# Kernel tuning notes

Measured on AMD Instinct MI355X. Metric: run time of the kernel, lower is better.

Reference implementation:

```python
import jax, jax.numpy as jnp
import numpy as np

N, E = 100000, 600000
IN_DIM, HID, OUT_DIM = 128, 128, 1
BN_EPS = 1e-5
L2_EPS = 1e-12


def setup_inputs() -> dict:
    key = jax.random.key(0)
    ks = jax.random.split(key, 12)

    def xavier(k, shape):
        fan_in, fan_out = shape[0], shape[1]
        lim = float(np.sqrt(6.0 / (fan_in + fan_out)))
        return jax.random.uniform(k, shape, jnp.float32, -lim, lim)

    return {
        'x': jax.random.normal(ks[0], (N, IN_DIM), jnp.float32),
        'edge_index': jax.random.randint(ks[1], (2, E), 0, N, jnp.int32),
        # SAGEConv layer 1: lin_l (neighbor, with bias), lin_r (root, no bias)
        'W1_l': xavier(ks[2], (IN_DIM, HID)),
        'b1_l': jnp.zeros((HID,), jnp.float32),
        'W1_r': xavier(ks[3], (IN_DIM, HID)),
        # BatchNorm1d(hidden)
        'bn_gamma': jnp.ones((HID,), jnp.float32),
        'bn_beta': jnp.zeros((HID,), jnp.float32),
        # SAGEConv layer 2
        'W2_l': xavier(ks[4], (HID, HID)),
        'b2_l': jnp.zeros((HID,), jnp.float32),
        'W2_r': xavier(ks[5], (HID, HID)),
        # fc on causal half of embedding
        'fc_W': xavier(ks[6], (HID // 2, OUT_DIM)),
        'fc_b': jnp.zeros((OUT_DIM,), jnp.float32),
    }


def _sage_conv(x, src, dst, W_l, b_l, W_r, n_nodes):
    # mean-aggregate neighbor features: messages x[src] scattered to dst
    msg = x[src]  # [E, d] gather
    agg = jax.ops.segment_sum(msg, dst, num_segments=n_nodes)  # [N, d]
    cnt = jax.ops.segment_sum(jnp.ones((src.shape[0],), x.dtype), dst,
                              num_segments=n_nodes)  # [N]
    mean = agg / jnp.maximum(cnt, 1.0)[:, None]
    out = mean @ W_l + b_l + x @ W_r  # lin_l(agg) + lin_r(x)
    # normalize=True -> row-wise L2 normalize (F.normalize, eps=1e-12)
    nrm = jnp.linalg.norm(out, axis=-1, keepdims=True)
    return out / jnp.maximum(nrm, L2_EPS)


def reference(x, edge_index, W1_l, b1_l, W1_r, bn_gamma, bn_beta,
              W2_l, b2_l, W2_r, fc_W, fc_b):
    src, dst = edge_index[0], edge_index[1]
    n_nodes = x.shape[0]

    h = _sage_conv(x, src, dst, W1_l, b1_l, W1_r, n_nodes)

    # transition: ReLU -> BatchNorm1d (batch stats) -> Dropout (eval: identity)
    h = jax.nn.relu(h)
    mu = jnp.mean(h, axis=0)
    var = jnp.var(h, axis=0)
    h = (h - mu) * jax.lax.rsqrt(var + BN_EPS) * bn_gamma + bn_beta

    embed = _sage_conv(h, src, dst, W2_l, b2_l, W2_r, n_nodes)

    half = embed.shape[1] // 2
    preds = (embed[:, :half] @ fc_W + fc_b).squeeze()  # [N]
    return preds, embed
```

## Files before the change

### kernel.cpp

```cpp
#include <hip/hip_runtime.h>
#include <hip/hip_bf16.h>
#include <stdint.h>

typedef __attribute__((ext_vector_type(8))) __bf16 bf16x8;
typedef __attribute__((ext_vector_type(4))) float  f32x4;

__device__ __forceinline__ float bflo(uint32_t p){ return __uint_as_float(p << 16); }
__device__ __forceinline__ float bfhi(uint32_t p){ return __uint_as_float(p & 0xffff0000u); }
__device__ __forceinline__ uint16_t f2bf(float f){
    uint32_t u = __float_as_uint(f);
    uint32_t r = (u + 0x7fffu + ((u >> 16) & 1u)) >> 16;
    return (uint16_t)r;
}
__device__ __forceinline__ uint32_t packbf(float a, float b){
    return (uint32_t)f2bf(a) | ((uint32_t)f2bf(b) << 16);
}
__device__ __forceinline__ f32x4 MFMA(bf16x8 a, bf16x8 b, f32x4 c){
    return __builtin_amdgcn_mfma_f32_16x16x32_bf16(a, b, c, 0, 0, 0);
}


__global__ void k_deg(const int* __restrict__ dst, int* __restrict__ counts, int E){
    int e = blockIdx.x * 256 + threadIdx.x;
    if (e < E) atomicAdd(&counts[dst[e]], 1);
}

__global__ void k_scan1(const int* __restrict__ counts, int* __restrict__ bsums, int N){
    __shared__ int lds[256];
    int t = threadIdx.x;
    int base = blockIdx.x * 2048 + t * 8;
    int s = 0;
    #pragma unroll
    for (int i = 0; i < 8; ++i){ int idx = base + i; s += (idx < N) ? counts[idx] : 0; }
    lds[t] = s; __syncthreads();
    for (int off = 128; off > 0; off >>= 1){
        if (t < off) lds[t] += lds[t + off];
        __syncthreads();
    }
    if (t == 0) bsums[blockIdx.x] = lds[0];
}

__global__ void k_scan2(int* bsums, int NB){
    int run = 0;
    for (int i = 0; i < NB; ++i){ int v = bsums[i]; bsums[i] = run; run += v; }
}

__global__ void k_scan3(const int* __restrict__ counts, const int* __restrict__ bsums,
                        int* __restrict__ offs, int N){
    __shared__ int lds[256];
    int t = threadIdx.x;
    int base = blockIdx.x * 2048 + t * 8;
    int local[8];
    int s = 0;
    #pragma unroll
    for (int i = 0; i < 8; ++i){
        int idx = base + i;
        int v = (idx < N) ? counts[idx] : 0;
        local[i] = v; s += v;
    }
    lds[t] = s; __syncthreads();
    for (int off = 1; off < 256; off <<= 1){
        int v = (t >= off) ? lds[t - off] : 0;
        __syncthreads();
        lds[t] += v;
        __syncthreads();
    }
    int run = bsums[blockIdx.x] + (lds[t] - s);
    #pragma unroll
    for (int i = 0; i < 8; ++i){
        int idx = base + i;
        if (idx < N){ offs[idx] = run; run += local[i]; }
    }
}

__global__ void k_fill(const int* __restrict__ src, const int* __restrict__ dst,
                       const int* __restrict__ offs, int* __restrict__ cursor,
                       int* __restrict__ ssrc, int E){
    int e = blockIdx.x * 256 + threadIdx.x;
    if (e < E){
        int d = dst[e];
        int p = atomicAdd(&cursor[d], 1);
        ssrc[offs[d] + p] = src[e];
    }
}

__global__ __launch_bounds__(256) void k_x2bf(const float* __restrict__ X,
        uint32_t* __restrict__ XbfE, uint32_t* __restrict__ Xlo, int N){
    int i = blockIdx.x * 256 + threadIdx.x;
    if (i >= N * 32) return;
    int row = i >> 5, l = i & 31;
    float4 v = *(const float4*)(X + (size_t)i * 4);
    uint16_t h0 = f2bf(v.x), h1 = f2bf(v.y), h2 = f2bf(v.z), h3 = f2bf(v.w);
    float r0 = v.x - __uint_as_float((uint32_t)h0 << 16);
    float r1 = v.y - __uint_as_float((uint32_t)h1 << 16);
    float r2 = v.z - __uint_as_float((uint32_t)h2 << 16);
    float r3 = v.w - __uint_as_float((uint32_t)h3 << 16);
    uint2 hi; hi.x = (uint32_t)h0 | ((uint32_t)h1 << 16);
    hi.y = (uint32_t)h2 | ((uint32_t)h3 << 16);
    uint2 lo; lo.x = packbf(r0, r1); lo.y = packbf(r2, r3);
    *(uint2*)(XbfE + (size_t)row * 128 + l * 2) = hi;
    *(uint2*)(Xlo  + (size_t)row * 64  + l * 2) = lo;
}

__global__ void k_wprep(const float* __restrict__ Wl, const float* __restrict__ Wr,
                        const float* __restrict__ scale,
                        uint16_t* __restrict__ Wpk){
    int idx = blockIdx.x * 256 + threadIdx.x;
    int c = idx >> 8, k = idx & 255;
    float v;
    if (k < 128){
        v = Wl[k * 128 + c];
    } else {
        v = Wr[(k - 128) * 128 + c];
        if (scale) v *= scale[k - 128];
    }
    uint16_t h = f2bf(v);
    float r = v - __uint_as_float((uint32_t)h << 16);
    int kt = k >> 5, kk = k & 31;
    int g = kk >> 3, e = kk & 7;
    int slot = (c << 2) | (g ^ ((c >> 1) & 3));
    size_t base = (size_t)kt * 8192 + (size_t)slot * 8 + e;
    Wpk[base]        = h;
    Wpk[base + 4096] = f2bf(r);
}

template<int MODE>
__global__ __launch_bounds__(256) void k_agg(
        const uint32_t* __restrict__ Src, int sstr,
        const int* __restrict__ offs, const int* __restrict__ counts,
        const int* __restrict__ ssrc,
        const float* __restrict__ bnscale, const float* __restrict__ bnshift,
        uint32_t* __restrict__ MbBase, int N){
    const int lane = threadIdx.x & 63;
    const int l15  = lane & 15;
    const int q    = lane >> 4;
    int node = blockIdx.x * 4 + (threadIdx.x >> 6);
    if (node >= N) return;
    int cnt = counts[node];
    if (cnt < 0) cnt = 0;
    int off = offs[node];
    const uint32_t* srcb = Src + l15 * 4;
    float a[8];
    #pragma unroll
    for (int i = 0; i < 8; ++i) a[i] = 0.f;

    int j = 0;
    for (; j + 8 <= cnt; j += 8){
        int s0 = ssrc[off + j + q];
        int s1 = ssrc[off + j + 4 + q];
        s0 = (s0 < 0) ? 0 : ((s0 >= N) ? (N - 1) : s0);
        s1 = (s1 < 0) ? 0 : ((s1 >= N) ? (N - 1) : s1);
        uint4 v0 = *(const uint4*)(srcb + (size_t)s0 * sstr);
        uint4 v1 = *(const uint4*)(srcb + (size_t)s1 * sstr);
        a[0] += bflo(v0.x) + bflo(v1.x); a[1] += bfhi(v0.x) + bfhi(v1.x);
        a[2] += bflo(v0.y) + bflo(v1.y); a[3] += bfhi(v0.y) + bfhi(v1.y);
        a[4] += bflo(v0.z) + bflo(v1.z); a[5] += bfhi(v0.z) + bfhi(v1.z);
        a[6] += bflo(v0.w) + bflo(v1.w); a[7] += bfhi(v0.w) + bfhi(v1.w);
    }
    int rem = cnt - j;
    if (rem > 0){
        if (q < rem){
            int s0 = ssrc[off + j + q];
            s0 = (s0 < 0) ? 0 : ((s0 >= N) ? (N - 1) : s0);
            uint4 v0 = *(const uint4*)(srcb + (size_t)s0 * sstr);
            a[0] += bflo(v0.x); a[1] += bfhi(v0.x);
            a[2] += bflo(v0.y); a[3] += bfhi(v0.y);
            a[4] += bflo(v0.z); a[5] += bfhi(v0.z);
            a[6] += bflo(v0.w); a[7] += bfhi(v0.w);
        }
        if (rem > 4 && q < rem - 4){
            int s1 = ssrc[off + j + 4 + q];
            s1 = (s1 < 0) ? 0 : ((s1 >= N) ? (N - 1) : s1);
            uint4 v1 = *(const uint4*)(srcb + (size_t)s1 * sstr);
            a[0] += bflo(v1.x); a[1] += bfhi(v1.x);
            a[2] += bflo(v1.y); a[3] += bfhi(v1.y);
            a[4] += bflo(v1.z); a[5] += bfhi(v1.z);
            a[6] += bflo(v1.w); a[7] += bfhi(v1.w);
        }
    }

    #pragma unroll
    for (int i = 0; i < 8; ++i){
        a[i] += __shfl_xor(a[i], 16, 64);
        a[i] += __shfl_xor(a[i], 32, 64);
    }
    float inv = 1.0f / fmaxf((float)cnt, 1.0f);
    #pragma unroll
    for (int i = 0; i < 8; ++i) a[i] *= inv;

    if (MODE == 1){
        if (cnt > 0){
            int c0 = l15 * 8;
            float4 sc0 = *(const float4*)(bnscale + c0);
            float4 sc1 = *(const float4*)(bnscale + c0 + 4);
            float4 sh0 = *(const float4*)(bnshift + c0);
            float4 sh1 = *(const float4*)(bnshift + c0 + 4);
            a[0] = a[0] * sc0.x + sh0.x; a[1] = a[1] * sc0.y + sh0.y;
            a[2] = a[2] * sc0.z + sh0.z; a[3] = a[3] * sc0.w + sh0.w;
            a[4] = a[4] * sc1.x + sh1.x; a[5] = a[5] * sc1.y + sh1.y;
            a[6] = a[6] * sc1.z + sh1.z; a[7] = a[7] * sc1.w + sh1.w;
        } else {
            #pragma unroll
            for (int i = 0; i < 8; ++i) a[i] = 0.f;
        }
    }

    if (q == 0){
        uint4 o;
        o.x = packbf(a[0], a[1]); o.y = packbf(a[2], a[3]);
        o.z = packbf(a[4], a[5]); o.w = packbf(a[6], a[7]);
        *(uint4*)(MbBase + (size_t)node * 128 + 64 + l15 * 4) = o;
    }
}

__device__ __forceinline__ void stage4(const uint32_t* Wpk, uint32_t (*sB)[2048],
                                       int wid, int lane, int sel, int half){
    #pragma unroll
    for (int i = 0; i < 4; ++i){
        int ch = wid * 4 + i;
        int ktv = ch >> 3, part = ch & 7;
        __builtin_amdgcn_global_load_lds(
            Wpk + (size_t)(half * 4 + ktv) * 4096 + sel * 2048 + part * 256 + lane * 4,
            &sB[ktv][part * 256], 16, 0, 0);
    }
}

template<int MODE>
__global__ __launch_bounds__(512, 4) void k_gemm(
        const uint32_t* Own,
        const uint32_t* OwnLo,
        const uint32_t* Mb,
        const uint32_t* __restrict__ Wpk,
        const float* __restrict__ bias,
        uint32_t* HbfOut,
        float* Emb,
        float* __restrict__ bnsum, float* __restrict__ bnsumsq,
        const float* __restrict__ fcW, const float* __restrict__ fcb,
        float* __restrict__ preds, int N){
    __shared__ uint32_t __align__(16) sB[4][2048];
    const int lane = threadIdx.x & 63;
    const int wid  = threadIdx.x >> 6;
    const int l15  = lane & 15;
    const int g    = lane >> 4;
    const int gx4  = (g ^ ((l15 >> 1) & 3)) * 4;
    const int ostr = (MODE == 0) ? 128 : 64;
    const int wrow = blockIdx.x * 128 + wid * 16;

    stage4(Wpk, sB, wid, lane, 0, 0);

    int ar0 = wrow + l15; if (ar0 >= N) ar0 = N - 1;

    const uint32_t* mp0 = Mb  + (size_t)ar0 * 128 + 64 + g * 4;
    const uint32_t* op0 = Own + (size_t)ar0 * ostr + g * 4;

    bf16x8 am[4], ao[4];
    #pragma unroll
    for (int kq = 0; kq < 4; ++kq){
        am[kq] = *(const bf16x8*)(mp0 + kq * 16);
        ao[kq] = *(const bf16x8*)(op0 + kq * 16);
    }
    bf16x8 xl[4];
    if (MODE == 0){
        #pragma unroll
        for (int kq = 0; kq < 4; ++kq)
            xl[kq] = *(const bf16x8*)(OwnLo + (size_t)ar0 * 64 + g * 4 + kq * 16);
    }

    f32x4 acc[8];
    const f32x4 zero = {0.f, 0.f, 0.f, 0.f};
    #pragma unroll
    for (int t = 0; t < 8; ++t) acc[t] = zero;

#define COMPUTE4(AM, ADD_XLO)                                                 \
    _Pragma("unroll")                                                         \
    for (int kk = 0; kk < 4; ++kk){                                           \
        _Pragma("unroll")                                                     \
        for (int t = 0; t < 8; ++t){                                          \
            bf16x8 bq = *(const bf16x8*)(&sB[kk][(t * 16 + l15) * 16 + gx4]); \
            acc[t] = MFMA(AM[kk], bq, acc[t]);                                \
            if (ADD_XLO) acc[t] = MFMA(xl[kk], bq, acc[t]);                   \
        }                                                                     \
    }

    __syncthreads();
    COMPUTE4(am, false);
    __syncthreads();
    stage4(Wpk, sB, wid, lane, 0, 1);
    __syncthreads();
    COMPUTE4(ao, (MODE == 0));
    __syncthreads();
    stage4(Wpk, sB, wid, lane, 1, 0);
    __syncthreads();
    COMPUTE4(am, false);
    __syncthreads();
    stage4(Wpk, sB, wid, lane, 1, 1);
    __syncthreads();
    COMPUTE4(ao, false);
#undef COMPUTE4

    float bv[8];
    #pragma unroll
    for (int t = 0; t < 8; ++t) bv[t] = bias[t * 16 + l15];

    float fw[4]; float fb = 0.f;
    if (MODE == 1){
        #pragma unroll
        for (int t = 0; t < 4; ++t) fw[t] = fcW[t * 16 + l15];
        fb = fcb[0];
    }

    float pbs[8], pbq[8];
    #pragma unroll
    for (int t = 0; t < 8; ++t){ pbs[t] = 0.f; pbq[t] = 0.f; }

    #pragma unroll
    for (int j = 0; j < 4; ++j){
        int orow = wrow + 4 * g + j;
        bool valid = orow < N;
        float o[8]; float ss = 0.f;
        #pragma unroll
        for (int t = 0; t < 8; ++t){
            o[t] = acc[t][j] + bv[t];
            ss += o[t] * o[t];
        }
        ss += __shfl_xor(ss, 1, 64);
        ss += __shfl_xor(ss, 2, 64);
        ss += __shfl_xor(ss, 4, 64);
        ss += __shfl_xor(ss, 8, 64);
        float inv = 1.0f / fmaxf(sqrtf(ss), 1e-12f);
        if (MODE == 0){
            #pragma unroll
            for (int t = 0; t < 8; ++t){
                float v = fmaxf(o[t] * inv, 0.f);
                float pv = __shfl_xor(v, 1, 64);
                if (valid){
                    pbs[t] += v; pbq[t] += v * v;
                    if (!(lane & 1))
                        HbfOut[(size_t)orow * 64 + t * 8 + (l15 >> 1)] = packbf(v, pv);
                }
            }
        } else {
            float p = 0.f;
            #pragma unroll
            for (int t = 0; t < 8; ++t){
                float v = o[t] * inv;
                if (valid) Emb[(size_t)orow * 128 + t * 16 + l15] = v;
                if (t < 4) p += v * fw[t];
            }
            p += __shfl_xor(p, 1, 64);
            p += __shfl_xor(p, 2, 64);
            p += __shfl_xor(p, 4, 64);
            p += __shfl_xor(p, 8, 64);
            if (valid && l15 == 0) preds[orow] = p + fb;
        }
    }

    if (MODE == 0){
        float* lsum = (float*)&sB[0][0];
        float* lsq  = lsum + 128;
        #pragma unroll
        for (int t = 0; t < 8; ++t){
            pbs[t] += __shfl_xor(pbs[t], 16, 64);
            pbs[t] += __shfl_xor(pbs[t], 32, 64);
            pbq[t] += __shfl_xor(pbq[t], 16, 64);
            pbq[t] += __shfl_xor(pbq[t], 32, 64);
        }
        __syncthreads();
        if (threadIdx.x < 128){ lsum[threadIdx.x] = 0.f; lsq[threadIdx.x] = 0.f; }
        __syncthreads();
        if (lane < 16){
            #pragma unroll
            for (int t = 0; t < 8; ++t){
                atomicAdd(&lsum[t * 16 + lane], pbs[t]);
                atomicAdd(&lsq [t * 16 + lane], pbq[t]);
            }
        }
        __syncthreads();
        if (threadIdx.x < 128){
            atomicAdd(&bnsum[threadIdx.x],   lsum[threadIdx.x]);
            atomicAdd(&bnsumsq[threadIdx.x], lsq[threadIdx.x]);
        }
    }
}

__global__ void k_bnfinal(const float* __restrict__ bnsum, const float* __restrict__ bnsumsq,
                          const float* __restrict__ gamma, const float* __restrict__ beta,
                          const float* __restrict__ W2r, const float* __restrict__ b2,
                          float* __restrict__ scale, float* __restrict__ shift,
                          float* __restrict__ bias2, int N){
    __shared__ float sh_l[128];
    int t = threadIdx.x;
    float invN = 1.0f / (float)N;
    float mu  = bnsum[t] * invN;
    float var = fmaxf(bnsumsq[t] * invN - mu * mu, 0.f);
    float istd = 1.0f / sqrtf(var + 1e-5f);
    float sc = gamma[t] * istd;
    float sf = beta[t] - mu * sc;
    scale[t] = sc; shift[t] = sf; sh_l[t] = sf;
    __syncthreads();
    float acc = b2[t];
    for (int k = 0; k < 128; ++k) acc += sh_l[k] * W2r[k * 128 + t];
    bias2[t] = acc;
}

__global__ void k_sent(float* __restrict__ preds, int N, float val){
    int i = blockIdx.x * 256 + threadIdx.x;
    if (i < N) preds[i] = val;
}

extern "C" void kernel_launch(void* const* d_in, const int* in_sizes, int n_in,
                              void* d_out, int out_size, void* d_ws, size_t ws_size,
                              hipStream_t stream){
    const int N = in_sizes[0] / 128;
    const int E = in_sizes[1] / 2;

    const float* x    = (const float*)d_in[0];
    const int*   ei   = (const int*)d_in[1];
    const int*   src  = ei;
    const int*   dst  = ei + E;
    const float* W1l  = (const float*)d_in[2];
    const float* b1   = (const float*)d_in[3];
    const float* W1r  = (const float*)d_in[4];
    const float* gam  = (const float*)d_in[5];
    const float* bet  = (const float*)d_in[6];
    const float* W2l  = (const float*)d_in[7];
    const float* b2   = (const float*)d_in[8];
    const float* W2r  = (const float*)d_in[9];
    const float* fcW  = (const float*)d_in[10];
    const float* fcb  = (const float*)d_in[11];

    float* preds = (float*)d_out;
    float* Emb   = preds + N;
    uint32_t* EmbU = (uint32_t*)Emb;

    char* w = (char*)d_ws;
    auto carve = [&](size_t bytes){ char* p = w; w += (bytes + 255) & ~(size_t)255; return p; };
    int*   counts  = (int*)  carve((size_t)N * 8);
    int*   cursor  = counts + N;
    int*   offs    = (int*)  carve((size_t)N * 4);
    int*   bsums   = (int*)  carve(256 * 4);
    float* bnsum   = (float*)carve(128 * 4);
    float* bnsumsq = (float*)carve(128 * 4);
    float* bnscale = (float*)carve(128 * 4);
    float* bnshift = (float*)carve(128 * 4);
    float* bias2   = (float*)carve(128 * 4);
    int*   ssrc    = (int*)  carve((size_t)E * 4);
    uint32_t* HbfXlo = (uint32_t*)carve((size_t)N * 256);
    uint16_t* Wpk1 = (uint16_t*)carve(131072);
    uint16_t* Wpk2 = (uint16_t*)carve(131072);
    size_t need = (size_t)(w - (char*)d_ws);
    if (ws_size < need){
        float val = 1024.f + 4.f * (float)((ws_size >> 20) > 255 ? 255 : (ws_size >> 20));
        k_sent<<<(N + 255) / 256, 256, 0, stream>>>(preds, N, val);
        return;
    }

    hipMemsetAsync(counts, 0, (size_t)N * 8, stream);
    hipMemsetAsync(bnsum,  0, 1024, stream);

    const int eb = (E + 255) / 256;
    const int NB = (N + 2047) / 2048;
    const int ab = (N + 3) / 4;
    const int gb = (N + 127) / 128;
    const int xb = (N * 32 + 255) / 256;

    k_deg  <<<eb, 256, 0, stream>>>(dst, counts, E);
    k_scan1<<<NB, 256, 0, stream>>>(counts, bsums, N);
    k_scan2<<<1,    1, 0, stream>>>(bsums, NB);
    k_scan3<<<NB, 256, 0, stream>>>(counts, bsums, offs, N);
    k_fill <<<eb, 256, 0, stream>>>(src, dst, offs, cursor, ssrc, E);

    k_x2bf <<<xb, 256, 0, stream>>>(x, EmbU, HbfXlo, N);
    k_wprep<<<128, 256, 0, stream>>>(W1l, W1r, nullptr, Wpk1);

    k_agg<0> <<<ab, 256, 0, stream>>>(EmbU, 128, offs, counts, ssrc,
                                      nullptr, nullptr, EmbU, N);
    k_gemm<0><<<gb, 512, 0, stream>>>(EmbU, HbfXlo, EmbU, (const uint32_t*)Wpk1, b1,
                                      HbfXlo, nullptr, bnsum, bnsumsq,
                                      nullptr, nullptr, nullptr, N);
    k_bnfinal<<<1, 128, 0, stream>>>(bnsum, bnsumsq, gam, bet, W2r, b2,
                                     bnscale, bnshift, bias2, N);
    k_wprep<<<128, 256, 0, stream>>>(W2l, W2r, bnscale, Wpk2);

    k_agg<1> <<<ab, 256, 0, stream>>>(HbfXlo, 64, offs, counts, ssrc,
                                      bnscale, bnshift, EmbU, N);
    k_gemm<1><<<gb, 512, 0, stream>>>(HbfXlo, nullptr, EmbU, (const uint32_t*)Wpk2, bias2,
                                      nullptr, Emb, nullptr, nullptr,
                                      fcW, fcb, preds, N);
}
```

Measured before the change: 356.5 us.

## Fuse neighbor mean aggregation into the SAGE GEMM kernel via LDS staging

Removes the separate k_agg kernels. Each GEMM warp now gathers and averages neighbor features for its own 16 rows, then writes the packed bf16 means into a swizzled LDS tile that feeds the MFMA A operand. This drops the global write and re-read of the mean buffer and two kernel launches. To fit, the GEMM block shrinks from 512 to 256 threads (64 rows per block), and each wave stages twice as much weight data. The cost is that each warp walks its 16 rows one after another, so fewer gather loads are in flight to hide memory latency.

Result: slower. 430.7 us (+20.8%).

```diff
diff --git a/kernel.cpp b/kernel.cpp
--- a/kernel.cpp
+++ b/kernel.cpp
@@ -124,100 +124,11 @@
     Wpk[base + 4096] = f2bf(r);
 }
 
-template<int MODE>
-__global__ __launch_bounds__(256) void k_agg(
-        const uint32_t* __restrict__ Src, int sstr,
-        const int* __restrict__ offs, const int* __restrict__ counts,
-        const int* __restrict__ ssrc,
-        const float* __restrict__ bnscale, const float* __restrict__ bnshift,
-        uint32_t* __restrict__ MbBase, int N){
-    const int lane = threadIdx.x & 63;
-    const int l15  = lane & 15;
-    const int q    = lane >> 4;
-    int node = blockIdx.x * 4 + (threadIdx.x >> 6);
-    if (node >= N) return;
-    int cnt = counts[node];
-    if (cnt < 0) cnt = 0;
-    int off = offs[node];
-    const uint32_t* srcb = Src + l15 * 4;
-    float a[8];
-    #pragma unroll
-    for (int i = 0; i < 8; ++i) a[i] = 0.f;
-
-    int j = 0;
-    for (; j + 8 <= cnt; j += 8){
-        int s0 = ssrc[off + j + q];
-        int s1 = ssrc[off + j + 4 + q];
-        s0 = (s0 < 0) ? 0 : ((s0 >= N) ? (N - 1) : s0);
-        s1 = (s1 < 0) ? 0 : ((s1 >= N) ? (N - 1) : s1);
-        uint4 v0 = *(const uint4*)(srcb + (size_t)s0 * sstr);
-        uint4 v1 = *(const uint4*)(srcb + (size_t)s1 * sstr);
-        a[0] += bflo(v0.x) + bflo(v1.x); a[1] += bfhi(v0.x) + bfhi(v1.x);
-        a[2] += bflo(v0.y) + bflo(v1.y); a[3] += bfhi(v0.y) + bfhi(v1.y);
-        a[4] += bflo(v0.z) + bflo(v1.z); a[5] += bfhi(v0.z) + bfhi(v1.z);
-        a[6] += bflo(v0.w) + bflo(v1.w); a[7] += bfhi(v0.w) + bfhi(v1.w);
-    }
-    int rem = cnt - j;
-    if (rem > 0){
-        if (q < rem){
-            int s0 = ssrc[off + j + q];
-            s0 = (s0 < 0) ? 0 : ((s0 >= N) ? (N - 1) : s0);
-            uint4 v0 = *(const uint4*)(srcb + (size_t)s0 * sstr);
-            a[0] += bflo(v0.x); a[1] += bfhi(v0.x);
-            a[2] += bflo(v0.y); a[3] += bfhi(v0.y);
-            a[4] += bflo(v0.z); a[5] += bfhi(v0.z);
-            a[6] += bflo(v0.w); a[7] += bfhi(v0.w);
-        }
-        if (rem > 4 && q < rem - 4){
-            int s1 = ssrc[off + j + 4 + q];
-            s1 = (s1 < 0) ? 0 : ((s1 >= N) ? (N - 1) : s1);
-            uint4 v1 = *(const uint4*)(srcb + (size_t)s1 * sstr);
-            a[0] += bflo(v1.x); a[1] += bfhi(v1.x);
-            a[2] += bflo(v1.y); a[3] += bfhi(v1.y);
-            a[4] += bflo(v1.z); a[5] += bfhi(v1.z);
-            a[6] += bflo(v1.w); a[7] += bfhi(v1.w);
-        }
-    }
-
-    #pragma unroll
-    for (int i = 0; i < 8; ++i){
-        a[i] += __shfl_xor(a[i], 16, 64);
-        a[i] += __shfl_xor(a[i], 32, 64);
-    }
-    float inv = 1.0f / fmaxf((float)cnt, 1.0f);
-    #pragma unroll
-    for (int i = 0; i < 8; ++i) a[i] *= inv;
-
-    if (MODE == 1){
-        if (cnt > 0){
-            int c0 = l15 * 8;
-            float4 sc0 = *(const float4*)(bnscale + c0);
-            float4 sc1 = *(const float4*)(bnscale + c0 + 4);
-            float4 sh0 = *(const float4*)(bnshift + c0);
-            float4 sh1 = *(const float4*)(bnshift + c0 + 4);
-            a[0] = a[0] * sc0.x + sh0.x; a[1] = a[1] * sc0.y + sh0.y;
-            a[2] = a[2] * sc0.z + sh0.z; a[3] = a[3] * sc0.w + sh0.w;
-            a[4] = a[4] * sc1.x + sh1.x; a[5] = a[5] * sc1.y + sh1.y;
-            a[6] = a[6] * sc1.z + sh1.z; a[7] = a[7] * sc1.w + sh1.w;
-        } else {
-            #pragma unroll
-            for (int i = 0; i < 8; ++i) a[i] = 0.f;
-        }
-    }
-
-    if (q == 0){
-        uint4 o;
-        o.x = packbf(a[0], a[1]); o.y = packbf(a[2], a[3]);
-        o.z = packbf(a[4], a[5]); o.w = packbf(a[6], a[7]);
-        *(uint4*)(MbBase + (size_t)node * 128 + 64 + l15 * 4) = o;
-    }
-}
-
 __device__ __forceinline__ void stage4(const uint32_t* Wpk, uint32_t (*sB)[2048],
                                        int wid, int lane, int sel, int half){
     #pragma unroll
-    for (int i = 0; i < 4; ++i){
-        int ch = wid * 4 + i;
+    for (int i = 0; i < 8; ++i){
+        int ch = wid * 8 + i;
         int ktv = ch >> 3, part = ch & 7;
         __builtin_amdgcn_global_load_lds(
             Wpk + (size_t)(half * 4 + ktv) * 4096 + sel * 2048 + part * 256 + lane * 4,
@@ -226,10 +137,12 @@
 }
 
 template<int MODE>
-__global__ __launch_bounds__(512, 4) void k_gemm(
+__global__ __launch_bounds__(256) void k_gemm(
         const uint32_t* Own,
         const uint32_t* OwnLo,
-        const uint32_t* Mb,
+        const int* __restrict__ offs, const int* __restrict__ counts,
+        const int* __restrict__ ssrc,
+        const float* __restrict__ bnscale, const float* __restrict__ bnshift,
         const uint32_t* __restrict__ Wpk,
         const float* __restrict__ bias,
         uint32_t* HbfOut,
@@ -238,27 +151,23 @@
         const float* __restrict__ fcW, const float* __restrict__ fcb,
         float* __restrict__ preds, int N){
     __shared__ uint32_t __align__(16) sB[4][2048];
+    __shared__ uint32_t __align__(16) sM[4][16][64];
     const int lane = threadIdx.x & 63;
     const int wid  = threadIdx.x >> 6;
     const int l15  = lane & 15;
     const int g    = lane >> 4;
     const int gx4  = (g ^ ((l15 >> 1) & 3)) * 4;
     const int ostr = (MODE == 0) ? 128 : 64;
-    const int wrow = blockIdx.x * 128 + wid * 16;
+    const int wrow = blockIdx.x * 64 + wid * 16;
 
     stage4(Wpk, sB, wid, lane, 0, 0);
 
     int ar0 = wrow + l15; if (ar0 >= N) ar0 = N - 1;
 
-    const uint32_t* mp0 = Mb  + (size_t)ar0 * 128 + 64 + g * 4;
     const uint32_t* op0 = Own + (size_t)ar0 * ostr + g * 4;
-
-    bf16x8 am[4], ao[4];
-    #pragma unroll
-    for (int kq = 0; kq < 4; ++kq){
-        am[kq] = *(const bf16x8*)(mp0 + kq * 16);
-        ao[kq] = *(const bf16x8*)(op0 + kq * 16);
-    }
+    bf16x8 ao[4];
+    #pragma unroll
+    for (int kq = 0; kq < 4; ++kq) ao[kq] = *(const bf16x8*)(op0 + kq * 16);
     bf16x8 xl[4];
     if (MODE == 0){
         #pragma unroll
@@ -266,37 +175,131 @@
             xl[kq] = *(const bf16x8*)(OwnLo + (size_t)ar0 * 64 + g * 4 + kq * 16);
     }
 
+    int cntv = counts[ar0];
+    int offv = offs[ar0];
+
+    float sc[8], sh[8];
+    if (MODE == 1){
+        int c0 = l15 * 8;
+        float4 s0 = *(const float4*)(bnscale + c0);
+        float4 s1 = *(const float4*)(bnscale + c0 + 4);
+        float4 h0 = *(const float4*)(bnshift + c0);
+        float4 h1 = *(const float4*)(bnshift + c0 + 4);
+        sc[0]=s0.x; sc[1]=s0.y; sc[2]=s0.z; sc[3]=s0.w;
+        sc[4]=s1.x; sc[5]=s1.y; sc[6]=s1.z; sc[7]=s1.w;
+        sh[0]=h0.x; sh[1]=h0.y; sh[2]=h0.z; sh[3]=h0.w;
+        sh[4]=h1.x; sh[5]=h1.y; sh[6]=h1.z; sh[7]=h1.w;
+    }
+
+    const uint32_t* srcb = Own + l15 * 4;
+    for (int r = 0; r < 16; ++r){
+        int cnt = __shfl(cntv, r, 64);
+        int off = __shfl(offv, r, 64);
+        if (cnt < 0) cnt = 0;
+        float a[8];
+        #pragma unroll
+        for (int i = 0; i < 8; ++i) a[i] = 0.f;
+        int j = 0;
+        for (; j + 8 <= cnt; j += 8){
+            int s0 = ssrc[off + j + g];
+            int s1 = ssrc[off + j + 4 + g];
+            s0 = (s0 < 0) ? 0 : ((s0 >= N) ? (N - 1) : s0);
+            s1 = (s1 < 0) ? 0 : ((s1 >= N) ? (N - 1) : s1);
+            uint4 v0 = *(const uint4*)(srcb + (size_t)s0 * ostr);
+            uint4 v1 = *(const uint4*)(srcb + (size_t)s1 * ostr);
+            a[0] += bflo(v0.x) + bflo(v1.x); a[1] += bfhi(v0.x) + bfhi(v1.x);
+            a[2] += bflo(v0.y) + bflo(v1.y); a[3] += bfhi(v0.y) + bfhi(v1.y);
+            a[4] += bflo(v0.z) + bflo(v1.z); a[5] += bfhi(v0.z) + bfhi(v1.z);
+            a[6] += bflo(v0.w) + bflo(v1.w); a[7] += bfhi(v0.w) + bfhi(v1.w);
+        }
+        int rem = cnt - j;
+        if (rem > 0){
+            if (g < rem){
+                int s0 = ssrc[off + j + g];
+                s0 = (s0 < 0) ? 0 : ((s0 >= N) ? (N - 1) : s0);
+                uint4 v0 = *(const uint4*)(srcb + (size_t)s0 * ostr);
+                a[0] += bflo(v0.x); a[1] += bfhi(v0.x);
+                a[2] += bflo(v0.y); a[3] += bfhi(v0.y);
+                a[4] += bflo(v0.z); a[5] += bfhi(v0.z);
+                a[6] += bflo(v0.w); a[7] += bfhi(v0.w);
+            }
+            if (rem > 4 && g < rem - 4){
+                int s1 = ssrc[off + j + 4 + g];
+                s1 = (s1 < 0) ? 0 : ((s1 >= N) ? (N - 1) : s1);
+                uint4 v1 = *(const uint4*)(srcb + (size_t)s1 * ostr);
+                a[0] += bflo(v1.x); a[1] += bfhi(v1.x);
+                a[2] += bflo(v1.y); a[3] += bfhi(v1.y);
+                a[4] += bflo(v1.z); a[5] += bfhi(v1.z);
+                a[6] += bflo(v1.w); a[7] += bfhi(v1.w);
+            }
+        }
+        #pragma unroll
+        for (int i = 0; i < 8; ++i){
+            a[i] += __shfl_xor(a[i], 16, 64);
+            a[i] += __shfl_xor(a[i], 32, 64);
+        }
+        float inv = 1.0f / fmaxf((float)cnt, 1.0f);
+        #pragma unroll
+        for (int i = 0; i < 8; ++i) a[i] *= inv;
+        if (MODE == 1){
+            if (cnt > 0){
+                #pragma unroll
+                for (int i = 0; i < 8; ++i) a[i] = a[i] * sc[i] + sh[i];
+            } else {
+                #pragma unroll
+                for (int i = 0; i < 8; ++i) a[i] = 0.f;
+            }
+        }
+        if (g == 0){
+            uint4 o;
+            o.x = packbf(a[0], a[1]); o.y = packbf(a[2], a[3]);
+            o.z = packbf(a[4], a[5]); o.w = packbf(a[6], a[7]);
+            *(uint4*)&sM[wid][r][(l15 ^ (r & 7)) * 4] = o;
+        }
+    }
+
     f32x4 acc[8];
     const f32x4 zero = {0.f, 0.f, 0.f, 0.f};
     #pragma unroll
     for (int t = 0; t < 8; ++t) acc[t] = zero;
 
-#define COMPUTE4(AM, ADD_XLO)                                                 \
+#define COMPUTE_MEAN()                                                        \
+    _Pragma("unroll")                                                         \
+    for (int kk = 0; kk < 4; ++kk){                                           \
+        bf16x8 aq = *(const bf16x8*)&sM[wid][l15][((kk * 4 + g) ^ (l15 & 7)) * 4]; \
+        _Pragma("unroll")                                                     \
+        for (int t = 0; t < 8; ++t){                                          \
+            bf16x8 bq = *(const bf16x8*)(&sB[kk][(t * 16 + l15) * 16 + gx4]); \
+            acc[t] = MFMA(aq, bq, acc[t]);                                    \
+        }                                                                     \
+    }
+#define COMPUTE_OWN(ADD_XLO)                                                  \
     _Pragma("unroll")                                                         \
     for (int kk = 0; kk < 4; ++kk){                                           \
         _Pragma("unroll")                                                     \
         for (int t = 0; t < 8; ++t){                                          \
             bf16x8 bq = *(const bf16x8*)(&sB[kk][(t * 16 + l15) * 16 + gx4]); \
-            acc[t] = MFMA(AM[kk], bq, acc[t]);                                \
+            acc[t] = MFMA(ao[kk], bq, acc[t]);                                \
             if (ADD_XLO) acc[t] = MFMA(xl[kk], bq, acc[t]);                   \
         }                                                                     \
     }
 
     __syncthreads();
-    COMPUTE4(am, false);
+    COMPUTE_MEAN();
     __syncthreads();
     stage4(Wpk, sB, wid, lane, 0, 1);
     __syncthreads();
-    COMPUTE4(ao, (MODE == 0));
+    COMPUTE_OWN((MODE == 0));
     __syncthreads();
     stage4(Wpk, sB, wid, lane, 1, 0);
     __syncthreads();
-    COMPUTE4(am, false);
+    COMPUTE_MEAN();
     __syncthreads();
     stage4(Wpk, sB, wid, lane, 1, 1);
     __syncthreads();
-    COMPUTE4(ao, false);
-#undef COMPUTE4
+    COMPUTE_OWN(false);
+#undef COMPUTE_MEAN
+#undef COMPUTE_OWN
 
     float bv[8];
     #pragma unroll
@@ -460,8 +463,7 @@
 
     const int eb = (E + 255) / 256;
     const int NB = (N + 2047) / 2048;
-    const int ab = (N + 3) / 4;
-    const int gb = (N + 127) / 128;
+    const int gb = (N + 63) / 64;
     const int xb = (N * 32 + 255) / 256;
 
     k_deg  <<<eb, 256, 0, stream>>>(dst, counts, E);
@@ -473,18 +475,18 @@
     k_x2bf <<<xb, 256, 0, stream>>>(x, EmbU, HbfXlo, N);
     k_wprep<<<128, 256, 0, stream>>>(W1l, W1r, nullptr, Wpk1);
 
-    k_agg<0> <<<ab, 256, 0, stream>>>(EmbU, 128, offs, counts, ssrc,
-                                      nullptr, nullptr, EmbU, N);
-    k_gemm<0><<<gb, 512, 0, stream>>>(EmbU, HbfXlo, EmbU, (const uint32_t*)Wpk1, b1,
+    k_gemm<0><<<gb, 256, 0, stream>>>(EmbU, HbfXlo, offs, counts, ssrc,
+                                      nullptr, nullptr,
+                                      (const uint32_t*)Wpk1, b1,
                                       HbfXlo, nullptr, bnsum, bnsumsq,
                                       nullptr, nullptr, nullptr, N);
     k_bnfinal<<<1, 128, 0, stream>>>(bnsum, bnsumsq, gam, bet, W2r, b2,
                                      bnscale, bnshift, bias2, N);
     k_wprep<<<128, 256, 0, stream>>>(W2l, W2r, bnscale, Wpk2);
 
-    k_agg<1> <<<ab, 256, 0, stream>>>(HbfXlo, 64, offs, counts, ssrc,
-                                      bnscale, bnshift, EmbU, N);
-    k_gemm<1><<<gb, 512, 0, stream>>>(HbfXlo, nullptr, EmbU, (const uint32_t*)Wpk2, bias2,
+    k_gemm<1><<<gb, 256, 0, stream>>>(HbfXlo, nullptr, offs, counts, ssrc,
+                                      bnscale, bnshift,
+                                      (const uint32_t*)Wpk2, bias2,
                                       nullptr, Emb, nullptr, nullptr,
                                       fcW, fcb, preds, N);
 }
```
